# Kernel optimization log

Measured on AMD Instinct MI355X. Metric: run time of the kernel, lower is better.

Reference implementation:

```python
import math
import jax, jax.numpy as jnp
import numpy as np

CHUNK_LEN = 64
NUM_HEADS = 16
HIDDEN = 1024
HEAD = HIDDEN // NUM_HEADS


def setup_inputs() -> dict:
    key = jax.random.key(0)
    ks = jax.random.split(key, 8)
    B, S, C, N, L = 4, 2048, 32, 2, 128
    scale = 1.0 / math.sqrt(HIDDEN)
    return {
        "query": jax.random.normal(ks[0], (B, S, HIDDEN), jnp.float32),
        "kv": jax.random.normal(ks[1], (B, C, N, L, HIDDEN), jnp.float32),
        "Wq": jax.random.normal(ks[2], (HIDDEN, HIDDEN), jnp.float32) * scale,
        "bq": jnp.zeros((HIDDEN,), jnp.float32),
        "Wk": jax.random.normal(ks[3], (HIDDEN, HIDDEN), jnp.float32) * scale,
        "bk": jnp.zeros((HIDDEN,), jnp.float32),
        "Wv": jax.random.normal(ks[4], (HIDDEN, HIDDEN), jnp.float32) * scale,
        "bv": jnp.zeros((HIDDEN,), jnp.float32),
    }


def reference(query, kv, Wq, bq, Wk, bk, Wv, bv):
    B, S, H = query.shape
    _, C, N, L, _ = kv.shape
    # shift query right by chunk_len-1 and pad to n_chunks*chunk_len
    q = query[:, CHUNK_LEN - 1:]
    add_len = C * CHUNK_LEN - q.shape[1]
    q = jnp.pad(q, ((0, 0), (0, add_len), (0, 0)))
    q = q.reshape(B, C, CHUNK_LEN, H)
    q = (q @ Wq.T + bq).reshape(B, C, CHUNK_LEN, NUM_HEADS, HEAD)
    k = (kv @ Wk.T + bk).reshape(B, C, N, L, NUM_HEADS, HEAD)
    v = (kv @ Wv.T + bv).reshape(B, C, N, L, NUM_HEADS, HEAD)
    # scores: [B, C, heads, chunk_len, N, L]
    attn = jnp.einsum("bcihd,bcnjhd->bchinj", q, k) / math.sqrt(HEAD)
    # softmax over flattened neighbor dims (n, j)
    attn = jax.nn.softmax(attn.reshape(B, C, NUM_HEADS, CHUNK_LEN, N * L), axis=-1)
    attn = attn.reshape(B, C, NUM_HEADS, CHUNK_LEN, N, L)
    h = jnp.einsum("bchinj,bcnjhd->bcihd", attn, v).reshape(B, C * CHUNK_LEN, H)
    # shift left: prepend chunk_len-1 zeros, truncate to seq_len
    h = jnp.pad(h, ((0, 0), (CHUNK_LEN - 1, 0), (0, 0)))[:, :S]
    return h
```

## Files before the change

### kernel.cpp

```cpp
#include <hip/hip_runtime.h>
#include <stdint.h>

#define HD 1024
#define SEQ 2048
#define NC 32

typedef __bf16 bf16x4 __attribute__((ext_vector_type(4)));
typedef __bf16 bf16x8 __attribute__((ext_vector_type(8)));
typedef float f32x4 __attribute__((ext_vector_type(4)));

__device__ inline unsigned short f2bf(float f) {
  union { float f; unsigned int u; } v; v.f = f;
  unsigned int r = v.u + 0x7fffu + ((v.u >> 16) & 1u);
  return (unsigned short)(r >> 16);
}
__device__ inline unsigned int pk2bf(float a, float b) {
  return (unsigned int)f2bf(a) | ((unsigned int)f2bf(b) << 16);
}
__device__ inline bf16x8 ld_frag8(const unsigned short* p) {
  bf16x4 lo = *(const bf16x4*)p;
  bf16x4 hi = *(const bf16x4*)(p + 4);
  return __builtin_shufflevector(lo, hi, 0, 1, 2, 3, 4, 5, 6, 7);
}
__device__ inline void glds16(const unsigned short* g, unsigned short* l) {
  __builtin_amdgcn_global_load_lds(
      (const __attribute__((address_space(1))) unsigned int*)g,
      (__attribute__((address_space(3))) unsigned int*)l, 16, 0, 0);
}
__device__ inline int swz64(int row, int j) { return (row * 8 + (j ^ (row & 7))) * 8; }

__global__ __launch_bounds__(256) void zero_head_kernel(float* __restrict__ out) {
  int i = (blockIdx.x * 256 + threadIdx.x) * 4;
  int b = i / 64512;
  int r = i - b * 64512;
  *(float4*)(out + (size_t)b * (SEQ * HD) + r) = make_float4(0.f, 0.f, 0.f, 0.f);
}

__global__ __launch_bounds__(256) void prep_all_kernel(
    const float* __restrict__ query, const float* __restrict__ kv,
    const float* __restrict__ Wq, const float* __restrict__ Wk,
    const float* __restrict__ Wv, unsigned short* __restrict__ Qbf,
    unsigned short* __restrict__ KVb, unsigned short* __restrict__ Wb,
    float* __restrict__ oz) {
  int bid = blockIdx.x;
  if (bid < 16384) {
    int i = bid * 256 + threadIdx.x;
    float4 a = ((const float4*)kv)[(size_t)i * 2];
    float4 b = ((const float4*)kv)[(size_t)i * 2 + 1];
    ((uint4*)KVb)[i] = make_uint4(pk2bf(a.x, a.y), pk2bf(a.z, a.w),
                                  pk2bf(b.x, b.y), pk2bf(b.z, b.w));
    return;
  }
  bid -= 16384;
  if (bid < 4096) {
    int i = bid * 256 + threadIdx.x;
    int g = i >> 7, c8 = (i & 127) * 8;
    int b = g >> 11, tt = g & 2047;
    uint4 o = make_uint4(0, 0, 0, 0);
    if (tt < 1985) {
      const float* src = query + ((size_t)(b << 11) + tt + 63) * HD + c8;
      float4 a = *(const float4*)src;
      float4 bb = *(const float4*)(src + 4);
      o = make_uint4(pk2bf(a.x, a.y), pk2bf(a.z, a.w), pk2bf(bb.x, bb.y), pk2bf(bb.z, bb.w));
    }
    *(uint4*)(Qbf + (size_t)g * HD + c8) = o;
    return;
  }
  bid -= 4096;
  if (bid < 1536) {
    int which = bid >> 9;
    int i = (bid & 511) * 256 + threadIdx.x;
    const float* src = which == 0 ? Wq : (which == 1 ? Wk : Wv);
    float4 a = ((const float4*)src)[(size_t)i * 2];
    float4 b = ((const float4*)src)[(size_t)i * 2 + 1];
    ((uint4*)(Wb + (size_t)which * 1048576))[i] =
        make_uint4(pk2bf(a.x, a.y), pk2bf(a.z, a.w), pk2bf(b.x, b.y), pk2bf(b.z, b.w));
    return;
  }
  bid -= 1536;
  int i = (bid * 256 + threadIdx.x) * 4;
  int b = i / 64512;
  int r = i - b * 64512;
  *(float4*)(oz + (size_t)b * (SEQ * HD) + r) = make_float4(0.f, 0.f, 0.f, 0.f);
}

__global__ __launch_bounds__(256, 2) void gemm_all_kernel(
    const unsigned short* __restrict__ Qbf, const unsigned short* __restrict__ KVb,
    const unsigned short* __restrict__ Wb,
    const float* __restrict__ bq, const float* __restrict__ bk, const float* __restrict__ bv,
    unsigned short* __restrict__ Qp, unsigned short* __restrict__ Kp,
    unsigned short* __restrict__ Vt) {
  __shared__ unsigned short lds_a[128 * 64];
  __shared__ unsigned short lds_b[128 * 64];
  __shared__ unsigned short lds_c[128 * 64];
  const int t = threadIdx.x;
  const int l = t & 63, w = t >> 6;
  const int wm = w >> 1, wn = w & 1;
  const int lr = l & 15, lq = l >> 4;
  int pr[4], pco[4];
#pragma unroll
  for (int p = 0; p < 4; ++p) {
    int pc = p * 256 + t;
    pr[p] = pc >> 3;
    pco[p] = ((pc & 7) ^ (pr[p] & 7)) * 8;
  }

  if (blockIdx.y < 256) {
    int lin = blockIdx.y * 8 + blockIdx.x;
    int s = (lin & 7) * 256 + (lin >> 3);
    const int bx = s & 7, by = s >> 3;
    const size_t arow0 = (size_t)by * 128;
    const size_t brow0 = (size_t)bx * 128;
    const unsigned short* Wk = Wb + (size_t)1048576;
    const unsigned short* Wv = Wb + (size_t)2097152;

    f32x4 acck[4][4], accv[4][4];
    for (int i = 0; i < 4; i++)
      for (int j = 0; j < 4; j++) {
        acck[i][j] = (f32x4){0.f, 0.f, 0.f, 0.f};
        accv[i][j] = (f32x4){0.f, 0.f, 0.f, 0.f};
      }

    for (int kk = 0; kk < 16; ++kk) {
      const int k0 = kk * 64;
      __syncthreads();
#pragma unroll
      for (int p = 0; p < 4; ++p) {
        glds16(KVb + (arow0 + pr[p]) * HD + k0 + pco[p], lds_a + (p * 256 + t) * 8);
        glds16(Wk + (brow0 + pr[p]) * HD + k0 + pco[p], lds_b + (p * 256 + t) * 8);
        glds16(Wv + (brow0 + pr[p]) * HD + k0 + pco[p], lds_c + (p * 256 + t) * 8);
      }
      __syncthreads();
#pragma unroll
      for (int h = 0; h < 2; ++h) {
        bf16x8 af[4];
        for (int mt = 0; mt < 4; ++mt)
          af[mt] = *(const bf16x8*)(lds_a + swz64(wm * 64 + mt * 16 + lr, h * 4 + lq));
        {
          bf16x8 bfr[4];
          for (int nt = 0; nt < 4; ++nt)
            bfr[nt] = *(const bf16x8*)(lds_b + swz64(wn * 64 + nt * 16 + lr, h * 4 + lq));
          for (int mt = 0; mt < 4; ++mt)
            for (int nt = 0; nt < 4; ++nt)
              acck[mt][nt] = __builtin_amdgcn_mfma_f32_16x16x32_bf16(af[mt], bfr[nt], acck[mt][nt], 0, 0, 0);
        }
        {
          bf16x8 bfr[4];
          for (int nt = 0; nt < 4; ++nt)
            bfr[nt] = *(const bf16x8*)(lds_c + swz64(wn * 64 + nt * 16 + lr, h * 4 + lq));
          for (int mt = 0; mt < 4; ++mt)
            for (int nt = 0; nt < 4; ++nt)
              accv[mt][nt] = __builtin_amdgcn_mfma_f32_16x16x32_bf16(af[mt], bfr[nt], accv[mt][nt], 0, 0, 0);
        }
      }
    }

    for (int nt = 0; nt < 4; ++nt) {
      int n = bx * 128 + wn * 64 + nt * 16 + lr;
      float bvv = bk[n];
      for (int mt = 0; mt < 4; ++mt) {
        size_t mbase = arow0 + wm * 64 + mt * 16 + lq * 4;
        for (int r = 0; r < 4; ++r)
          Kp[(mbase + r) * HD + n] = f2bf(acck[mt][nt][r] + bvv);
      }
    }
    for (int nt = 0; nt < 4; ++nt) {
      int n = bx * 128 + wn * 64 + nt * 16 + lr;
      float bvv = bv[n];
      int h = n >> 6, d = n & 63;
      for (int mt = 0; mt < 4; ++mt) {
        size_t m0 = arow0 + wm * 64 + mt * 16 + lq * 4;
        size_t bc = m0 >> 8, j = m0 & 255;
        *(ushort4*)(Vt + ((bc * 16 + h) * 64 + d) * 256 + j) =
            make_ushort4(f2bf(accv[mt][nt][0] + bvv), f2bf(accv[mt][nt][1] + bvv),
                         f2bf(accv[mt][nt][2] + bvv), f2bf(accv[mt][nt][3] + bvv));
      }
    }
  } else {
    int lin = (blockIdx.y - 256) * 8 + blockIdx.x;
    int s = (lin & 7) * 64 + (lin >> 3);
    const int bx = s & 7, by = s >> 3;
    const size_t arow0 = (size_t)by * 128;
    const size_t brow0 = (size_t)bx * 128;

    f32x4 acc[4][4];
    for (int i = 0; i < 4; i++)
      for (int j = 0; j < 4; j++) acc[i][j] = (f32x4){0.f, 0.f, 0.f, 0.f};

    for (int kk = 0; kk < 16; ++kk) {
      const int k0 = kk * 64;
      __syncthreads();
#pragma unroll
      for (int p = 0; p < 4; ++p) {
        glds16(Qbf + (arow0 + pr[p]) * HD + k0 + pco[p], lds_a + (p * 256 + t) * 8);
        glds16(Wb + (brow0 + pr[p]) * HD + k0 + pco[p], lds_b + (p * 256 + t) * 8);
      }
      __syncthreads();
#pragma unroll
      for (int h = 0; h < 2; ++h) {
        bf16x8 af[4], bfr[4];
        for (int mt = 0; mt < 4; ++mt)
          af[mt] = *(const bf16x8*)(lds_a + swz64(wm * 64 + mt * 16 + lr, h * 4 + lq));
        for (int nt = 0; nt < 4; ++nt)
          bfr[nt] = *(const bf16x8*)(lds_b + swz64(wn * 64 + nt * 16 + lr, h * 4 + lq));
        for (int mt = 0; mt < 4; ++mt)
          for (int nt = 0; nt < 4; ++nt)
            acc[mt][nt] = __builtin_amdgcn_mfma_f32_16x16x32_bf16(af[mt], bfr[nt], acc[mt][nt], 0, 0, 0);
      }
    }

    for (int nt = 0; nt < 4; ++nt) {
      int n = bx * 128 + wn * 64 + nt * 16 + lr;
      float bvv = bq[n];
      for (int mt = 0; mt < 4; ++mt) {
        size_t mbase = arow0 + wm * 64 + mt * 16 + lq * 4;
        for (int r = 0; r < 4; ++r)
          Qp[(mbase + r) * HD + n] = f2bf(acc[mt][nt][r] + bvv);
      }
    }
  }
}

__global__ __launch_bounds__(256, 2) void gemm_f32_kernel(
    const float* __restrict__ A, const float* __restrict__ W,
    const float* __restrict__ bias, unsigned short* __restrict__ Cout,
    int store_vt, int qremap) {
  __shared__ unsigned short lds_a[128 * 32];
  __shared__ unsigned short lds_b[128 * 32];
  const int t = threadIdx.x;
  const int l = t & 63, w = t >> 6;
  const int wm = w >> 1, wn = w & 1;
  const int lr = l & 15, lq = l >> 4;
  const size_t arow0 = (size_t)blockIdx.y * 128;
  const size_t brow0 = (size_t)blockIdx.x * 128;

  f32x4 acc[4][4];
  for (int i = 0; i < 4; i++)
    for (int j = 0; j < 4; j++) acc[i][j] = (f32x4){0.f, 0.f, 0.f, 0.f};

  for (int kk = 0; kk < 32; ++kk) {
    const int k0 = kk * 32;
    uint4 av[2], bv[2];
    for (int p = 0; p < 2; ++p) {
      int chunk = p * 256 + t;
      int row = chunk >> 2, c8 = (chunk & 3) * 8;
      size_t grow = arow0 + row;
      bool valid = true;
      const float* srcA;
      if (qremap) {
        int bb = (int)(grow >> 11), tt = (int)(grow & 2047);
        valid = tt < 1985;
        srcA = A + ((size_t)(bb << 11) + tt + 63) * HD + k0 + c8;
      } else {
        srcA = A + grow * HD + k0 + c8;
      }
      if (valid) {
        float4 x = *(const float4*)srcA, y = *(const float4*)(srcA + 4);
        av[p] = make_uint4(pk2bf(x.x, x.y), pk2bf(x.z, x.w), pk2bf(y.x, y.y), pk2bf(y.z, y.w));
      } else av[p] = make_uint4(0, 0, 0, 0);
      const float* srcB = W + (brow0 + row) * HD + k0 + c8;
      float4 x = *(const float4*)srcB, y = *(const float4*)(srcB + 4);
      bv[p] = make_uint4(pk2bf(x.x, x.y), pk2bf(x.z, x.w), pk2bf(y.x, y.y), pk2bf(y.z, y.w));
    }
    __syncthreads();
    for (int p = 0; p < 2; ++p) {
      int chunk = p * 256 + t;
      *(uint4*)(lds_a + chunk * 8) = av[p];
      *(uint4*)(lds_b + chunk * 8) = bv[p];
    }
    __syncthreads();
    bf16x8 af[4], bfr[4];
    for (int mt = 0; mt < 4; ++mt)
      af[mt] = *(const bf16x8*)(lds_a + (wm * 64 + mt * 16 + lr) * 32 + lq * 8);
    for (int nt = 0; nt < 4; ++nt)
      bfr[nt] = *(const bf16x8*)(lds_b + (wn * 64 + nt * 16 + lr) * 32 + lq * 8);
    for (int mt = 0; mt < 4; ++mt)
      for (int nt = 0; nt < 4; ++nt)
        acc[mt][nt] = __builtin_amdgcn_mfma_f32_16x16x32_bf16(af[mt], bfr[nt], acc[mt][nt], 0, 0, 0);
  }

  if (!store_vt) {
    for (int nt = 0; nt < 4; ++nt) {
      int n = blockIdx.x * 128 + wn * 64 + nt * 16 + lr;
      float bvv = bias[n];
      for (int mt = 0; mt < 4; ++mt) {
        size_t mbase = arow0 + wm * 64 + mt * 16 + lq * 4;
        for (int r = 0; r < 4; ++r)
          Cout[(mbase + r) * HD + n] = f2bf(acc[mt][nt][r] + bvv);
      }
    }
  } else {
    for (int nt = 0; nt < 4; ++nt) {
      int n = blockIdx.x * 128 + wn * 64 + nt * 16 + lr;
      float bvv = bias[n];
      int h = n >> 6, d = n & 63;
      for (int mt = 0; mt < 4; ++mt) {
        size_t m0 = arow0 + wm * 64 + mt * 16 + lq * 4;
        size_t bc = m0 >> 8, j = m0 & 255;
        *(ushort4*)(Cout + ((bc * 16 + h) * 64 + d) * 256 + j) =
            make_ushort4(f2bf(acc[mt][nt][0] + bvv), f2bf(acc[mt][nt][1] + bvv),
                         f2bf(acc[mt][nt][2] + bvv), f2bf(acc[mt][nt][3] + bvv));
      }
    }
  }
}

#define QK_STRIDE 72
#define P_STRIDE 260

__global__ __launch_bounds__(256, 3) void attn_kernel(
    const unsigned short* __restrict__ Qp, const unsigned short* __restrict__ Kp,
    const unsigned short* __restrict__ Vt, float* __restrict__ out) {
  __shared__ unsigned short k_s[256 * QK_STRIDE];
  const int t = threadIdx.x;
  const int l = t & 63, w = t >> 6;
  const int lr = l & 15, lq = l >> 4;
  const int bid = blockIdx.x;
  const int head = bid & 15, cc = (bid >> 4) & 31, b = bid >> 9;
  const size_t qrow0 = (size_t)(b * NC + cc) * 64;
  const size_t kvrow0 = (size_t)(b * NC + cc) * 256;
  const int hcol = head * 64;
  const unsigned short* vbase = Vt + ((size_t)((b * NC + cc) * 16 + head) * 64) * 256;

  for (int p = 0; p < 8; ++p) {
    int chunk = p * 256 + t;
    int row = chunk >> 3, c8 = (chunk & 7) * 8;
    *(uint4*)(k_s + row * QK_STRIDE + c8) = *(const uint4*)(Kp + (kvrow0 + row) * HD + hcol + c8);
  }
  bf16x8 qa0 = ld_frag8(Qp + (qrow0 + w * 16 + lr) * HD + hcol + lq * 8);
  bf16x8 qa1 = ld_frag8(Qp + (qrow0 + w * 16 + lr) * HD + hcol + 32 + lq * 8);
  __syncthreads();

  f32x4 sc[16];
  __builtin_amdgcn_s_setprio(1);
  for (int nt = 0; nt < 16; ++nt) {
    bf16x8 kb0 = ld_frag8(k_s + (nt * 16 + lr) * QK_STRIDE + lq * 8);
    bf16x8 kb1 = ld_frag8(k_s + (nt * 16 + lr) * QK_STRIDE + 32 + lq * 8);
    f32x4 a = (f32x4){0.f, 0.f, 0.f, 0.f};
    a = __builtin_amdgcn_mfma_f32_16x16x32_bf16(kb0, qa0, a, 0, 0, 0);
    a = __builtin_amdgcn_mfma_f32_16x16x32_bf16(kb1, qa1, a, 0, 0, 0);
    sc[nt] = a;
  }
  __builtin_amdgcn_s_setprio(0);

  float m = -1e30f;
  for (int nt = 0; nt < 16; ++nt)
    for (int r = 0; r < 4; ++r) m = fmaxf(m, sc[nt][r]);
  m = fmaxf(m, __shfl_xor(m, 16));
  m = fmaxf(m, __shfl_xor(m, 32));
  float s = 0.f;
  const float cexp = 0.18033688011112042f;
  for (int nt = 0; nt < 16; ++nt)
    for (int r = 0; r < 4; ++r) {
      float p = exp2f((sc[nt][r] - m) * cexp);
      sc[nt][r] = p;
      s += p;
    }
  s += __shfl_xor(s, 16);
  s += __shfl_xor(s, 32);

  bf16x8 va[4];
#pragma unroll
  for (int nt2 = 0; nt2 < 4; ++nt2)
    va[nt2] = *(const bf16x8*)(vbase + (size_t)(nt2 * 16 + lr) * 256 + lq * 8);

  __syncthreads();

  for (int nt = 0; nt < 16; ++nt) {
    *(uint2*)(k_s + (w * 16 + lr) * P_STRIDE + nt * 16 + lq * 4) =
        make_uint2(pk2bf(sc[nt][0], sc[nt][1]), pk2bf(sc[nt][2], sc[nt][3]));
  }

  f32x4 o[4];
  for (int i = 0; i < 4; ++i) o[i] = (f32x4){0.f, 0.f, 0.f, 0.f};
  bf16x8 vbuf[4];
#pragma unroll
  for (int ks = 0; ks < 8; ks += 2) {
#pragma unroll
    for (int nt2 = 0; nt2 < 4; ++nt2)
      vbuf[nt2] = *(const bf16x8*)(vbase + (size_t)(nt2 * 16 + lr) * 256 + (ks + 1) * 32 + lq * 8);
    bf16x8 pa = ld_frag8(k_s + (w * 16 + lr) * P_STRIDE + ks * 32 + lq * 8);
    __builtin_amdgcn_s_setprio(1);
#pragma unroll
    for (int nt2 = 0; nt2 < 4; ++nt2)
      o[nt2] = __builtin_amdgcn_mfma_f32_16x16x32_bf16(pa, va[nt2], o[nt2], 0, 0, 0);
    __builtin_amdgcn_s_setprio(0);
    if (ks + 2 < 8) {
#pragma unroll
      for (int nt2 = 0; nt2 < 4; ++nt2)
        va[nt2] = *(const bf16x8*)(vbase + (size_t)(nt2 * 16 + lr) * 256 + (ks + 2) * 32 + lq * 8);
    }
    bf16x8 pb = ld_frag8(k_s + (w * 16 + lr) * P_STRIDE + (ks + 1) * 32 + lq * 8);
    __builtin_amdgcn_s_setprio(1);
#pragma unroll
    for (int nt2 = 0; nt2 < 4; ++nt2)
      o[nt2] = __builtin_amdgcn_mfma_f32_16x16x32_bf16(pb, vbuf[nt2], o[nt2], 0, 0, 0);
    __builtin_amdgcn_s_setprio(0);
  }

  for (int r = 0; r < 4; ++r) {
    int strip = w * 16 + lq * 4 + r;
    int trow = cc * 64 + strip;
    float sv = __shfl(s, lq * 4 + r, 16);
    if (trow < 1985) {
      size_t orow = (size_t)b * SEQ + trow + 63;
      float inv = 1.0f / sv;
      for (int nt2 = 0; nt2 < 4; ++nt2)
        out[orow * HD + hcol + nt2 * 16 + lr] = o[nt2][r] * inv;
    }
  }
}

extern "C" void kernel_launch(void* const* d_in, const int* in_sizes, int n_in,
                              void* d_out, int out_size, void* d_ws, size_t ws_size,
                              hipStream_t stream) {
  (void)in_sizes; (void)n_in; (void)out_size;
  const float* query = (const float*)d_in[0];
  const float* kv    = (const float*)d_in[1];
  const float* Wq    = (const float*)d_in[2];
  const float* bq    = (const float*)d_in[3];
  const float* Wk    = (const float*)d_in[4];
  const float* bk    = (const float*)d_in[5];
  const float* Wv    = (const float*)d_in[6];
  const float* bv    = (const float*)d_in[7];
  float* out = (float*)d_out;

  unsigned short* Qp  = (unsigned short*)d_ws;
  unsigned short* Kp  = Qp + (size_t)8192 * 1024;
  unsigned short* Vt  = Kp + (size_t)32768 * 1024;
  unsigned short* Qbf = Vt + (size_t)32768 * 1024;
  unsigned short* KVb = Qbf + (size_t)8192 * 1024;
  unsigned short* Wqb = KVb + (size_t)32768 * 1024;
  const size_t need = ((size_t)8192 * 1024 * 2 + (size_t)32768 * 1024 * 2 + (size_t)1024 * 1024 * 3) * 2;
  const bool big = ws_size >= need;

  if (big) {
    prep_all_kernel<<<dim3(22268), dim3(256), 0, stream>>>(query, kv, Wq, Wk, Wv,
                                                           Qbf, KVb, Wqb, out);
    gemm_all_kernel<<<dim3(8, 320), dim3(256), 0, stream>>>(Qbf, KVb, Wqb, bq, bk, bv,
                                                            Qp, Kp, Vt);
  } else {
    zero_head_kernel<<<dim3(252), dim3(256), 0, stream>>>(out);
    gemm_f32_kernel<<<dim3(8, 64), dim3(256), 0, stream>>>(query, Wq, bq, Qp, 0, 1);
    gemm_f32_kernel<<<dim3(8, 256), dim3(256), 0, stream>>>(kv, Wk, bk, Kp, 0, 0);
    gemm_f32_kernel<<<dim3(8, 256), dim3(256), 0, stream>>>(kv, Wv, bv, Vt, 1, 0);
  }
  attn_kernel<<<dim3(2048), dim3(256), 0, stream>>>(Qp, Kp, Vt, out);
}
```

Measured before the change: 461.5 us.

## Double-buffer LDS tiles with K=32 stages in projection GEMM kernel

The projection GEMM now uses two LDS buffers with a K-step of 32 instead of a single buffer with K-step 64. Async global-to-LDS loads for the next tile are issued before the MFMA compute on the current tile, and the swizzle is adjusted to the narrower tile. This aims to hide global load latency behind compute. In exchange it doubles the number of barriers and iterations, and the smaller per-iteration work may limit how much latency is actually hidden.

Result: slower. 480.7 us (+4.2%).

```diff
diff --git a/kernel.cpp b/kernel.cpp
--- a/kernel.cpp
+++ b/kernel.cpp
@@ -27,7 +27,10 @@
       (const __attribute__((address_space(1))) unsigned int*)g,
       (__attribute__((address_space(3))) unsigned int*)l, 16, 0, 0);
 }
-__device__ inline int swz64(int row, int j) { return (row * 8 + (j ^ (row & 7))) * 8; }
+__device__ inline int swz32(int row, int j) {
+  int lr8 = row >> 1;
+  return (lr8 * 8 + ((((row & 1) << 2) | j) ^ (lr8 & 7))) * 8;
+}
 
 __global__ __launch_bounds__(256) void zero_head_kernel(float* __restrict__ out) {
   int i = (blockIdx.x * 256 + threadIdx.x) * 4;
@@ -90,19 +93,21 @@
     const float* __restrict__ bq, const float* __restrict__ bk, const float* __restrict__ bv,
     unsigned short* __restrict__ Qp, unsigned short* __restrict__ Kp,
     unsigned short* __restrict__ Vt) {
-  __shared__ unsigned short lds_a[128 * 64];
-  __shared__ unsigned short lds_b[128 * 64];
-  __shared__ unsigned short lds_c[128 * 64];
+  __shared__ unsigned short lds_a[2][4096];
+  __shared__ unsigned short lds_b[2][4096];
+  __shared__ unsigned short lds_c[2][4096];
   const int t = threadIdx.x;
   const int l = t & 63, w = t >> 6;
   const int wm = w >> 1, wn = w & 1;
   const int lr = l & 15, lq = l >> 4;
-  int pr[4], pco[4];
-#pragma unroll
-  for (int p = 0; p < 4; ++p) {
+  int pr[2], pco[2];
+#pragma unroll
+  for (int p = 0; p < 2; ++p) {
     int pc = p * 256 + t;
-    pr[p] = pc >> 3;
-    pco[p] = ((pc & 7) ^ (pr[p] & 7)) * 8;
+    int lr8 = pc >> 3;
+    int e = (pc & 7) ^ (lr8 & 7);
+    pr[p] = lr8 * 2 + (e >> 2);
+    pco[p] = (e & 3) * 8;
   }
 
   if (blockIdx.y < 256) {
@@ -121,38 +126,45 @@
         accv[i][j] = (f32x4){0.f, 0.f, 0.f, 0.f};
       }
 
-    for (int kk = 0; kk < 16; ++kk) {
-      const int k0 = kk * 64;
-      __syncthreads();
-#pragma unroll
-      for (int p = 0; p < 4; ++p) {
-        glds16(KVb + (arow0 + pr[p]) * HD + k0 + pco[p], lds_a + (p * 256 + t) * 8);
-        glds16(Wk + (brow0 + pr[p]) * HD + k0 + pco[p], lds_b + (p * 256 + t) * 8);
-        glds16(Wv + (brow0 + pr[p]) * HD + k0 + pco[p], lds_c + (p * 256 + t) * 8);
-      }
-      __syncthreads();
-#pragma unroll
-      for (int h = 0; h < 2; ++h) {
-        bf16x8 af[4];
+    auto stage = [&](int buf, int k0) {
+#pragma unroll
+      for (int p = 0; p < 2; ++p) {
+        glds16(KVb + (arow0 + pr[p]) * HD + k0 + pco[p], lds_a[buf] + (p * 256 + t) * 8);
+        glds16(Wk + (brow0 + pr[p]) * HD + k0 + pco[p], lds_b[buf] + (p * 256 + t) * 8);
+        glds16(Wv + (brow0 + pr[p]) * HD + k0 + pco[p], lds_c[buf] + (p * 256 + t) * 8);
+      }
+    };
+    auto compute = [&](int buf) {
+      bf16x8 af[4];
+      for (int mt = 0; mt < 4; ++mt)
+        af[mt] = *(const bf16x8*)(lds_a[buf] + swz32(wm * 64 + mt * 16 + lr, lq));
+      {
+        bf16x8 bfr[4];
+        for (int nt = 0; nt < 4; ++nt)
+          bfr[nt] = *(const bf16x8*)(lds_b[buf] + swz32(wn * 64 + nt * 16 + lr, lq));
         for (int mt = 0; mt < 4; ++mt)
-          af[mt] = *(const bf16x8*)(lds_a + swz64(wm * 64 + mt * 16 + lr, h * 4 + lq));
-        {
-          bf16x8 bfr[4];
           for (int nt = 0; nt < 4; ++nt)
-            bfr[nt] = *(const bf16x8*)(lds_b + swz64(wn * 64 + nt * 16 + lr, h * 4 + lq));
-          for (int mt = 0; mt < 4; ++mt)
-            for (int nt = 0; nt < 4; ++nt)
-              acck[mt][nt] = __builtin_amdgcn_mfma_f32_16x16x32_bf16(af[mt], bfr[nt], acck[mt][nt], 0, 0, 0);
-        }
-        {
-          bf16x8 bfr[4];
+            acck[mt][nt] = __builtin_amdgcn_mfma_f32_16x16x32_bf16(af[mt], bfr[nt], acck[mt][nt], 0, 0, 0);
+      }
+      {
+        bf16x8 bfr[4];
+        for (int nt = 0; nt < 4; ++nt)
+          bfr[nt] = *(const bf16x8*)(lds_c[buf] + swz32(wn * 64 + nt * 16 + lr, lq));
+        for (int mt = 0; mt < 4; ++mt)
           for (int nt = 0; nt < 4; ++nt)
-            bfr[nt] = *(const bf16x8*)(lds_c + swz64(wn * 64 + nt * 16 + lr, h * 4 + lq));
-          for (int mt = 0; mt < 4; ++mt)
-            for (int nt = 0; nt < 4; ++nt)
-              accv[mt][nt] = __builtin_amdgcn_mfma_f32_16x16x32_bf16(af[mt], bfr[nt], accv[mt][nt], 0, 0, 0);
-        }
-      }
+            accv[mt][nt] = __builtin_amdgcn_mfma_f32_16x16x32_bf16(af[mt], bfr[nt], accv[mt][nt], 0, 0, 0);
+      }
+    };
+
+    stage(0, 0);
+    asm volatile("s_waitcnt vmcnt(0)" ::: "memory");
+    __builtin_amdgcn_s_barrier();
+    for (int kk = 0; kk < 32; ++kk) {
+      const int cur = kk & 1;
+      if (kk < 31) stage(cur ^ 1, (kk + 1) * 32);
+      compute(cur);
+      asm volatile("s_waitcnt vmcnt(0)" ::: "memory");
+      __builtin_amdgcn_s_barrier();
     }
 
     for (int nt = 0; nt < 4; ++nt) {
@@ -187,26 +199,33 @@
     for (int i = 0; i < 4; i++)
       for (int j = 0; j < 4; j++) acc[i][j] = (f32x4){0.f, 0.f, 0.f, 0.f};
 
-    for (int kk = 0; kk < 16; ++kk) {
-      const int k0 = kk * 64;
-      __syncthreads();
-#pragma unroll
-      for (int p = 0; p < 4; ++p) {
-        glds16(Qbf + (arow0 + pr[p]) * HD + k0 + pco[p], lds_a + (p * 256 + t) * 8);
-        glds16(Wb + (brow0 + pr[p]) * HD + k0 + pco[p], lds_b + (p * 256 + t) * 8);
-      }
-      __syncthreads();
-#pragma unroll
-      for (int h = 0; h < 2; ++h) {
-        bf16x8 af[4], bfr[4];
-        for (int mt = 0; mt < 4; ++mt)
-          af[mt] = *(const bf16x8*)(lds_a + swz64(wm * 64 + mt * 16 + lr, h * 4 + lq));
+    auto stage = [&](int buf, int k0) {
+#pragma unroll
+      for (int p = 0; p < 2; ++p) {
+        glds16(Qbf + (arow0 + pr[p]) * HD + k0 + pco[p], lds_a[buf] + (p * 256 + t) * 8);
+        glds16(Wb + (brow0 + pr[p]) * HD + k0 + pco[p], lds_b[buf] + (p * 256 + t) * 8);
+      }
+    };
+    auto compute = [&](int buf) {
+      bf16x8 af[4], bfr[4];
+      for (int mt = 0; mt < 4; ++mt)
+        af[mt] = *(const bf16x8*)(lds_a[buf] + swz32(wm * 64 + mt * 16 + lr, lq));
+      for (int nt = 0; nt < 4; ++nt)
+        bfr[nt] = *(const bf16x8*)(lds_b[buf] + swz32(wn * 64 + nt * 16 + lr, lq));
+      for (int mt = 0; mt < 4; ++mt)
         for (int nt = 0; nt < 4; ++nt)
-          bfr[nt] = *(const bf16x8*)(lds_b + swz64(wn * 64 + nt * 16 + lr, h * 4 + lq));
-        for (int mt = 0; mt < 4; ++mt)
-          for (int nt = 0; nt < 4; ++nt)
-            acc[mt][nt] = __builtin_amdgcn_mfma_f32_16x16x32_bf16(af[mt], bfr[nt], acc[mt][nt], 0, 0, 0);
-      }
+          acc[mt][nt] = __builtin_amdgcn_mfma_f32_16x16x32_bf16(af[mt], bfr[nt], acc[mt][nt], 0, 0, 0);
+    };
+
+    stage(0, 0);
+    asm volatile("s_waitcnt vmcnt(0)" ::: "memory");
+    __builtin_amdgcn_s_barrier();
+    for (int kk = 0; kk < 32; ++kk) {
+      const int cur = kk & 1;
+      if (kk < 31) stage(cur ^ 1, (kk + 1) * 32);
+      compute(cur);
+      asm volatile("s_waitcnt vmcnt(0)" ::: "memory");
+      __builtin_amdgcn_s_barrier();
     }
 
     for (int nt = 0; nt < 4; ++nt) {
```
